# Kernel optimization log

Hardware: AMD Instinct MI355X
Metric: run time of the kernel (lower is better)

Reference implementation:

```python
import jax, jax.numpy as jnp
import numpy as np

H = 32          # num attention heads
KVH = 8         # num kv heads
D = 64          # head dim
HID = 2048      # hidden size
MAXB = 1024     # max_bias_length
BASE = 10000.0  # rope theta


def _rope(x, pos):
    # x: (B, S, h, D), pos: (S,) -- GPT-NeoX half-split rotary
    half = D // 2
    inv_freq = 1.0 / (BASE ** (jnp.arange(0, D, 2, dtype=jnp.float32) / D))  # (half,)
    ang = pos[:, None].astype(jnp.float32) * inv_freq                         # (S, half)
    cos = jnp.cos(ang)[None, :, None, :]
    sin = jnp.sin(ang)[None, :, None, :]
    x1, x2 = x[..., :half], x[..., half:]
    return jnp.concatenate([x1 * cos - x2 * sin, x2 * cos + x1 * sin], axis=-1)


def setup_inputs() -> dict:
    key = jax.random.key(0)
    ks = jax.random.split(key, 7)
    B, S = 2, 1024
    hidden_states = jax.random.normal(ks[0], (B, S, HID), dtype=jnp.float32)
    attention_mask = jnp.broadcast_to(
        jnp.tril(jnp.ones((S, S), dtype=jnp.int32))[None, None], (B, 1, S, S))
    # weights stored as (in, out): y = x @ W  (same math as torch Linear)
    Wq = jax.random.normal(ks[1], (HID, H * D), dtype=jnp.float32) * 0.02
    Wk = jax.random.normal(ks[2], (HID, KVH * D), dtype=jnp.float32) * 0.02
    Wv = jax.random.normal(ks[3], (HID, KVH * D), dtype=jnp.float32) * 0.02
    Wo = jax.random.normal(ks[4], (H * D, HID), dtype=jnp.float32) * 0.02
    bias_diag = jax.random.normal(ks[5], (H, MAXB), dtype=jnp.float32) * 0.001
    softmax_offset = jnp.zeros((H,), dtype=jnp.float32)
    return {"hidden_states": hidden_states, "attention_mask": attention_mask,
            "Wq": Wq, "Wk": Wk, "Wv": Wv, "Wo": Wo,
            "bias_diag": bias_diag, "softmax_offset": softmax_offset}


def reference(hidden_states, attention_mask, Wq, Wk, Wv, Wo, bias_diag, softmax_offset):
    B, S, _ = hidden_states.shape
    scaling = D ** (-0.5)
    pos = jnp.arange(S)

    q = (hidden_states @ Wq).reshape(B, S, H, D)
    k = (hidden_states @ Wk).reshape(B, S, KVH, D)
    v = (hidden_states @ Wv).reshape(B, S, KVH, D)

    q = _rope(q, pos)
    k = _rope(k, pos)

    # (B, H, S, D); repeat_kv via repeat on head axis
    q = q.transpose(0, 2, 1, 3)
    k = jnp.repeat(k.transpose(0, 2, 1, 3), H // KVH, axis=1)
    v = jnp.repeat(v.transpose(0, 2, 1, 3), H // KVH, axis=1)

    scores = jnp.einsum('bhqd,bhkd->bhqk', q, k) * scaling

    # learnable diagonal relative-position bias
    rel = pos[:, None] - pos[None, :]                     # (S, S)
    valid = ((rel >= 0) & (rel < MAXB)).astype(scores.dtype)
    idx = jnp.clip(rel, 0, MAXB - 1)
    bias = bias_diag[:, idx] * valid                      # (H, S, S)
    scores = scores + bias[None]

    scores = jnp.where(attention_mask[:, :, :, :S] == 0, -jnp.inf, scores)

    weights = jax.nn.softmax(scores.astype(jnp.float32), axis=-1)

    # adaptive offset subtraction + relu
    offset = jnp.abs(softmax_offset + 1.0)[None, :, None, None]
    num_visible = (pos + 1).astype(jnp.float32)[None, None, :, None]  # along query dim
    weights = jax.nn.relu(weights - offset / num_visible)

    attn_out = jnp.einsum('bhqk,bhkd->bhqd', weights.astype(v.dtype), v)
    attn_out = attn_out.transpose(0, 2, 1, 3).reshape(B, S, H * D)
    return attn_out @ Wo
```

## Files before the change

kernel.cpp:

```cpp
#include <hip/hip_runtime.h>
#include <cstdint>
#include <cstddef>

#define BB   2
#define SS   1024
#define HID  2048
#define HH   32
#define KVHH 8
#define DD   64
#define NQKV 3072
#define QKW  2560

typedef __attribute__((ext_vector_type(8))) short bf16x8;
typedef __attribute__((ext_vector_type(4))) float f32x4;
typedef __attribute__((ext_vector_type(4))) unsigned int u32x4;

__device__ __forceinline__ unsigned short f2bf(float f) {
    unsigned int u = __float_as_uint(f);
    unsigned int r = (u + 0x7fffu + ((u >> 16) & 1u)) >> 16;
    return (unsigned short)r;
}

__device__ __forceinline__ void g2l16(const unsigned short* g, unsigned short* l) {
    __builtin_amdgcn_global_load_lds(
        (__attribute__((address_space(1))) void*)(unsigned short*)g,
        (__attribute__((address_space(3))) void*)l,
        16, 0, 0);
}

__global__ __launch_bounds__(256) void prep(
    const float* __restrict__ hidden,
    const float* __restrict__ Wq, const float* __restrict__ Wk,
    const float* __restrict__ Wv, const float* __restrict__ Wo,
    unsigned short* __restrict__ hidden_bf,
    unsigned short* __restrict__ WqkvT,
    unsigned short* __restrict__ WoT)
{
    const int z   = blockIdx.z;
    const int tid = threadIdx.x;

    if (z == 4) {
        int r0 = blockIdx.y * 64, c0 = blockIdx.x * 64;
        #pragma unroll
        for (int p = 0; p < 4; ++p) {
            int f = tid + p * 256;
            int row = r0 + (f >> 4), c4 = c0 + (f & 15) * 4;
            float4 v = *(const float4*)&hidden[(size_t)row * 2048 + c4];
            ushort4 o;
            o.x = f2bf(v.x); o.y = f2bf(v.y); o.z = f2bf(v.z); o.w = f2bf(v.w);
            *(ushort4*)&hidden_bf[(size_t)row * 2048 + c4] = o;
        }
        return;
    }

    const float* W;
    unsigned short* Wt;
    int N;
    if (z == 0)      { W = Wq; Wt = WqkvT;                        N = 2048; }
    else if (z == 1) { W = Wk; Wt = WqkvT + (size_t)2048 * 2048;  N = 512;  }
    else if (z == 2) { W = Wv; Wt = WqkvT + (size_t)2560 * 2048;  N = 512;  }
    else             { W = Wo; Wt = WoT;                          N = 2048; }
    if (blockIdx.x * 64 >= N) return;

    __shared__ float t[64][68];
    const int n0 = blockIdx.x * 64, k0 = blockIdx.y * 64;
    #pragma unroll
    for (int p = 0; p < 4; ++p) {
        int f = tid + p * 256;
        int row = f >> 4, c4 = (f & 15) * 4;
        float4 v = *(const float4*)&W[(size_t)(k0 + row) * N + n0 + c4];
        t[row][c4 + 0] = v.x; t[row][c4 + 1] = v.y;
        t[row][c4 + 2] = v.z; t[row][c4 + 3] = v.w;
    }
    __syncthreads();
    #pragma unroll
    for (int p = 0; p < 4; ++p) {
        int f = tid + p * 256;
        int nrow = f >> 4, kc4 = (f & 15) * 4;
        ushort4 o;
        o.x = f2bf(t[kc4 + 0][nrow]);
        o.y = f2bf(t[kc4 + 1][nrow]);
        o.z = f2bf(t[kc4 + 2][nrow]);
        o.w = f2bf(t[kc4 + 3][nrow]);
        *(ushort4*)&Wt[(size_t)(n0 + nrow) * 2048 + k0 + kc4] = o;
    }
}

__global__ __launch_bounds__(256) void gemm_qkv_fused(
    const unsigned short* __restrict__ A,
    const unsigned short* __restrict__ Bt,
    unsigned short* __restrict__ qk_bf,
    unsigned short* __restrict__ v_t)
{
    __shared__ __align__(16) char smem[49152];
    float* Ctf = (float*)smem;

    const int tid  = threadIdx.x;
    const int lane = tid & 63;
    const int wave = tid >> 6;
    const int quad = lane >> 4;
    const int l15  = lane & 15;
    const int wm = (wave >> 1) * 64, wn = (wave & 1) * 32;
    const int m0 = blockIdx.y * 128, n0 = blockIdx.x * 64;
    const int K = 2048;

    f32x4 acc[4][2] = {};

#define STAGE_Q(k0s, buf) do {                                                \
    unsigned short* Ad = (unsigned short*)(smem + (buf) * 24576);             \
    unsigned short* Bd = (unsigned short*)(smem + (buf) * 24576 + 16384);     \
    _Pragma("unroll")                                                         \
    for (int p = 0; p < 4; ++p) {                                             \
        int ci = tid + p * 256;                                               \
        int row_ = ci >> 3, sc_ = (ci & 7) ^ (row_ & 7);                      \
        g2l16(&A[(size_t)(m0 + row_) * K + (k0s) + sc_ * 8], Ad + ci * 8);    \
    }                                                                         \
    _Pragma("unroll")                                                         \
    for (int p = 0; p < 2; ++p) {                                             \
        int ci = tid + p * 256;                                               \
        int row_ = ci >> 3, sc_ = (ci & 7) ^ (row_ & 7);                      \
        g2l16(&Bt[(size_t)(n0 + row_) * K + (k0s) + sc_ * 8], Bd + ci * 8);   \
    } } while (0)

    STAGE_Q(0, 0);
    __syncthreads();
    int cur = 0;
    for (int k0 = 0; k0 < K; k0 += 64) {
        if (k0 + 64 < K) STAGE_Q(k0 + 64, cur ^ 1);
        const short* Ab = (const short*)(smem + cur * 24576);
        const short* Bb = (const short*)(smem + cur * 24576 + 16384);

        #pragma unroll
        for (int s = 0; s < 2; ++s) {
            bf16x8 af[4], bfr[2];
            #pragma unroll
            for (int i = 0; i < 4; ++i) {
                int row = wm + i * 16 + l15;
                af[i] = *(const bf16x8*)(Ab + row * 64 +
                        ((((s << 2) | quad) ^ (row & 7)) * 8));
            }
            #pragma unroll
            for (int j = 0; j < 2; ++j) {
                int row = wn + j * 16 + l15;
                bfr[j] = *(const bf16x8*)(Bb + row * 64 +
                        ((((s << 2) | quad) ^ (row & 7)) * 8));
            }
            #pragma unroll
            for (int i = 0; i < 4; ++i)
                #pragma unroll
                for (int j = 0; j < 2; ++j)
                    acc[i][j] = __builtin_amdgcn_mfma_f32_16x16x32_bf16(
                        af[i], bfr[j], acc[i][j], 0, 0, 0);
        }
        __syncthreads();
        cur ^= 1;
    }

    #pragma unroll
    for (int i = 0; i < 4; ++i)
        #pragma unroll
        for (int j = 0; j < 2; ++j)
            #pragma unroll
            for (int rg = 0; rg < 4; ++rg)
                Ctf[(wm + i * 16 + quad * 4 + rg) * 65 + wn + j * 16 + l15]
                    = acc[i][j][rg];
    __syncthreads();

    const int bx = blockIdx.x;
    const int b  = m0 >> 10;
    const int s0 = m0 & 1023;

    if (bx < 40) {
        const int hc = bx * 64;
        const float scale = (bx < 32) ? 0.125f : 1.0f;
        #pragma unroll
        for (int p = 0; p < 4; ++p) {
            int idx = tid + p * 256;
            int row = idx >> 3, t0 = (idx & 7) * 4;
            int s = s0 + row;
            ushort4 o1, o2;
            #pragma unroll
            for (int k = 0; k < 4; ++k) {
                int t = t0 + k;
                float x1 = Ctf[row * 65 + t];
                float x2 = Ctf[row * 65 + t + 32];
                float inv = __expf(-(float)t * 0.28782313662425572f);
                float ang = (float)s * inv;
                float c  = __cosf(ang);
                float sn = __sinf(ang);
                ((unsigned short*)&o1)[k] = f2bf((x1 * c - x2 * sn) * scale);
                ((unsigned short*)&o2)[k] = f2bf((x2 * c + x1 * sn) * scale);
            }
            unsigned short* dst = qk_bf + (size_t)(m0 + row) * QKW + hc;
            *(ushort4*)&dst[t0]      = o1;
            *(ushort4*)&dst[t0 + 32] = o2;
        }
    } else {
        const int vb = b * 512 + (bx - 40) * 64;
        #pragma unroll
        for (int p = 0; p < 8; ++p) {
            int idx = tid + p * 256;
            int c = idx >> 5, srow = (idx & 31) * 4;
            ushort4 o;
            #pragma unroll
            for (int k = 0; k < 4; ++k)
                ((unsigned short*)&o)[k] = f2bf(Ctf[(srow + k) * 65 + c]);
            *(ushort4*)&v_t[(size_t)(vb + c) * 1024 + s0 + srow] = o;
        }
    }
#undef STAGE_Q
}

__global__ __launch_bounds__(256) void gemm_bf16_bt(
    const unsigned short* __restrict__ A,
    const unsigned short* __restrict__ Bt,
    float* __restrict__ C, int M, int N, int K)
{
    __shared__ __align__(16) char smem[49152];

    const int tid  = threadIdx.x;
    const int lane = tid & 63;
    const int wave = tid >> 6;
    const int quad = lane >> 4;
    const int l15  = lane & 15;
    const int wm = (wave >> 1) * 64, wn = (wave & 1) * 32;
    const int m0 = blockIdx.y * 128, n0 = blockIdx.x * 64;

    f32x4 acc[4][2] = {};

#define STAGE_O(k0s, buf) do {                                                \
    unsigned short* Ad = (unsigned short*)(smem + (buf) * 24576);             \
    unsigned short* Bd = (unsigned short*)(smem + (buf) * 24576 + 16384);     \
    _Pragma("unroll")                                                         \
    for (int p = 0; p < 4; ++p) {                                             \
        int ci = tid + p * 256;                                               \
        int row_ = ci >> 3, sc_ = (ci & 7) ^ (row_ & 7);                      \
        g2l16(&A[(size_t)(m0 + row_) * K + (k0s) + sc_ * 8], Ad + ci * 8);    \
    }                                                                         \
    _Pragma("unroll")                                                         \
    for (int p = 0; p < 2; ++p) {                                             \
        int ci = tid + p * 256;                                               \
        int row_ = ci >> 3, sc_ = (ci & 7) ^ (row_ & 7);                      \
        g2l16(&Bt[(size_t)(n0 + row_) * K + (k0s) + sc_ * 8], Bd + ci * 8);   \
    } } while (0)

    STAGE_O(0, 0);
    __syncthreads();
    int cur = 0;
    for (int k0 = 0; k0 < K; k0 += 64) {
        if (k0 + 64 < K) STAGE_O(k0 + 64, cur ^ 1);
        const short* Ab = (const short*)(smem + cur * 24576);
        const short* Bb = (const short*)(smem + cur * 24576 + 16384);

        #pragma unroll
        for (int s = 0; s < 2; ++s) {
            bf16x8 af[4], bfr[2];
            #pragma unroll
            for (int i = 0; i < 4; ++i) {
                int row = wm + i * 16 + l15;
                af[i] = *(const bf16x8*)(Ab + row * 64 +
                        ((((s << 2) | quad) ^ (row & 7)) * 8));
            }
            #pragma unroll
            for (int j = 0; j < 2; ++j) {
                int row = wn + j * 16 + l15;
                bfr[j] = *(const bf16x8*)(Bb + row * 64 +
                        ((((s << 2) | quad) ^ (row & 7)) * 8));
            }
            #pragma unroll
            for (int i = 0; i < 4; ++i)
                #pragma unroll
                for (int j = 0; j < 2; ++j)
                    acc[i][j] = __builtin_amdgcn_mfma_f32_16x16x32_bf16(
                        af[i], bfr[j], acc[i][j], 0, 0, 0);
        }
        __syncthreads();
        cur ^= 1;
    }

    #pragma unroll
    for (int i = 0; i < 4; ++i) {
        int grow = m0 + wm + i * 16 + quad * 4;
        #pragma unroll
        for (int j = 0; j < 2; ++j) {
            int gcol = n0 + wn + j * 16 + l15;
            #pragma unroll
            for (int rg = 0; rg < 4; ++rg)
                C[(size_t)(grow + rg) * N + gcol] = acc[i][j][rg];
        }
    }
#undef STAGE_O
}

__global__ __launch_bounds__(512, 4) void attn_mfma(
    const unsigned short* __restrict__ qk_bf,
    const unsigned short* __restrict__ v_t,
    const float* __restrict__ bias_diag,
    const float* __restrict__ soff,
    unsigned short* __restrict__ AO)
{
    const int id = (int)blockIdx.x;
    const int h  = id & 31;
    const int b  = (id >> 5) & 1;
    const int pi = id >> 6;
    const int kh = h >> 2;
    const int tid  = threadIdx.x;
    const int lane = tid & 63;
    const int wave = tid >> 6;
    const int grp  = wave >> 2;
    const int w4   = wave & 3;
    const int gt   = tid & 255;
    const int quad = lane >> 4;
    const int l15  = lane & 15;

    __shared__ short Ks[2][2][4096];
    __shared__ short Vs[2][2][4096];
    __shared__ float bd_s[1024];
    __shared__ float red[2][64];

    for (int i = tid; i < 1024; i += 512) bd_s[i] = bias_diag[h * 1024 + i];

    const unsigned short* Kg = qk_bf + (size_t)(b * SS) * QKW + 2048 + kh * 64;
    const unsigned short* Vg = v_t + (size_t)(b * 512 + kh * 64) * SS;

    short* KsG = &Ks[grp][0][0];
    short* VsG = &Vs[grp][0][0];
    float* Fred = (float*)&Ks[1][0][0];

#define STAGE_K(j, buf) do {                                                  \
    _Pragma("unroll")                                                         \
    for (int p = 0; p < 2; ++p) {                                             \
        int ci = gt + p * 256;                                                \
        int row_ = ci >> 3;                                                   \
        int sc_  = (ci & 7) ^ (row_ & 7);                                     \
        g2l16(Kg + (size_t)((j) * 64 + row_) * QKW + sc_ * 8,                 \
              (unsigned short*)(KsG + (buf) * 4096 + ci * 8));                \
    } } while (0)

#define STAGE_V(j, buf) do {                                                  \
    _Pragma("unroll")                                                         \
    for (int p = 0; p < 2; ++p) {                                             \
        int ci = gt + p * 256;                                                \
        int row_ = ci >> 3;                                                   \
        int sc_  = (ci & 7) ^ (row_ & 7);                                     \
        g2l16(Vg + (size_t)row_ * SS + (j) * 64 + sc_ * 8,                    \
              (unsigned short*)(VsG + (buf) * 4096 + ci * 8));                \
    } } while (0)

    #pragma unroll 1
    for (int half = 0; half < 2; ++half) {
        const int qt = half ? pi : 15 - pi;
        const int q0 = qt * 64;
        const int nI = (qt + 2) >> 1;
        const int qrow = q0 + w4 * 16 + l15;

        const unsigned short* Qg =
            qk_bf + (size_t)(b * SS + q0 + w4 * 16) * QKW + h * 64;
        bf16x8 qf0 = *(const bf16x8*)(Qg + (size_t)l15 * QKW + quad * 8);
        bf16x8 qf1 = *(const bf16x8*)(Qg + (size_t)l15 * QKW + 32 + quad * 8);

        float lpa[4] = {0.f, 0.f, 0.f, 0.f};
        if (grp <= qt) STAGE_K(grp, 0);
        __syncthreads();
        int cur = 0;
        for (int i = 0; i < nI; ++i) {
            const int j = 2 * i + grp;
            if (j + 2 <= qt) STAGE_K(j + 2, cur ^ 1);
            if (j <= qt) {
                const short* Kb = KsG + cur * 4096;
                const bool diag = (j == qt);
                f32x4 acc[4] = {};
                #pragma unroll
                for (int nb = 0; nb < 4; ++nb) {
                    if (diag && nb > w4) continue;
                    int row = nb * 16 + l15, sw = row & 7;
                    bf16x8 a0 = *(const bf16x8*)(Kb + row * 64 + ((quad ^ sw) * 8));
                    bf16x8 a1 = *(const bf16x8*)(Kb + row * 64 + (((quad + 4) ^ sw) * 8));
                    acc[nb] = __builtin_amdgcn_mfma_f32_16x16x32_bf16(a0, qf0, acc[nb], 0, 0, 0);
                    acc[nb] = __builtin_amdgcn_mfma_f32_16x16x32_bf16(a1, qf1, acc[nb], 0, 0, 0);
                }
                if (!diag) {
                    #pragma unroll
                    for (int nb = 0; nb < 4; ++nb) {
                        int rel0 = qrow - (j * 64 + nb * 16 + quad * 4);
                        #pragma unroll
                        for (int r = 0; r < 4; ++r)
                            lpa[r] += __expf(acc[nb][r] + bd_s[rel0 - r]);
                    }
                } else {
                    #pragma unroll
                    for (int nb = 0; nb < 4; ++nb) {
                        if (nb > w4) continue;
                        #pragma unroll
                        for (int r = 0; r < 4; ++r) {
                            int rel = qrow - (j * 64 + nb * 16 + quad * 4 + r);
                            if (rel >= 0) lpa[r] += __expf(acc[nb][r] + bd_s[rel]);
                        }
                    }
                }
            }
            __syncthreads();
            cur ^= 1;
        }

        float lp = (lpa[0] + lpa[1]) + (lpa[2] + lpa[3]);
        lp += __shfl_xor(lp, 16, 64);
        lp += __shfl_xor(lp, 32, 64);
        if (quad == 0) red[grp][w4 * 16 + l15] = lp;
        __syncthreads();
        lp = red[0][w4 * 16 + l15] + red[1][w4 * 16 + l15];
        const float invl = 1.f / lp;
        const float cl   = fabsf(soff[h] + 1.f) / (float)(qrow + 1) * lp;

        f32x4 oacc[4] = {};
        if (grp <= qt) { STAGE_K(grp, 0); STAGE_V(grp, 0); }
        __syncthreads();
        cur = 0;
        for (int i = 0; i < nI; ++i) {
            const int j = 2 * i + grp;
            if (j + 2 <= qt) { STAGE_K(j + 2, cur ^ 1); STAGE_V(j + 2, cur ^ 1); }
            if (j <= qt) {
                const short* Kb = KsG + cur * 4096;
                const short* Vb = VsG + cur * 4096;
                const bool diag = (j == qt);

                f32x4 acc[4] = {};
                #pragma unroll
                for (int nb = 0; nb < 4; ++nb) {
                    if (diag && nb > w4) continue;
                    int row = nb * 16 + l15, sw = row & 7;
                    bf16x8 a0 = *(const bf16x8*)(Kb + row * 64 + ((quad ^ sw) * 8));
                    bf16x8 a1 = *(const bf16x8*)(Kb + row * 64 + (((quad + 4) ^ sw) * 8));
                    acc[nb] = __builtin_amdgcn_mfma_f32_16x16x32_bf16(a0, qf0, acc[nb], 0, 0, 0);
                    acc[nb] = __builtin_amdgcn_mfma_f32_16x16x32_bf16(a1, qf1, acc[nb], 0, 0, 0);
                }

                unsigned int pk[4][2];
                if (!diag) {
                    #pragma unroll
                    for (int nb = 0; nb < 4; ++nb) {
                        float w[4];
                        int rel0 = qrow - (j * 64 + nb * 16 + quad * 4);
                        #pragma unroll
                        for (int r = 0; r < 4; ++r)
                            w[r] = fmaxf(__expf(acc[nb][r] + bd_s[rel0 - r]) - cl, 0.f);
                        asm("v_cvt_pk_bf16_f32 %0, %1, %2" : "=v"(pk[nb][0]) : "v"(w[0]), "v"(w[1]));
                        asm("v_cvt_pk_bf16_f32 %0, %1, %2" : "=v"(pk[nb][1]) : "v"(w[2]), "v"(w[3]));
                    }
                } else {
                    #pragma unroll
                    for (int nb = 0; nb < 4; ++nb) {
                        float w[4];
                        #pragma unroll
                        for (int r = 0; r < 4; ++r) {
                            int rel = qrow - (j * 64 + nb * 16 + quad * 4 + r);
                            float e = 0.f;
                            if (rel >= 0)
                                e = fmaxf(__expf(acc[nb][r] + bd_s[rel]) - cl, 0.f);
                            w[r] = e;
                        }
                        asm("v_cvt_pk_bf16_f32 %0, %1, %2" : "=v"(pk[nb][0]) : "v"(w[0]), "v"(w[1]));
                        asm("v_cvt_pk_bf16_f32 %0, %1, %2" : "=v"(pk[nb][1]) : "v"(w[2]), "v"(w[3]));
                    }
                }
                unsigned int ppk[4][2];
                #pragma unroll
                for (int nb = 0; nb < 4; ++nb) {
                    ppk[nb][0] = __shfl_xor(pk[nb][0], 16, 64);
                    ppk[nb][1] = __shfl_xor(pk[nb][1], 16, 64);
                }

                const bool oddq = quad & 1;
                const int  cv   = ((quad & 1) << 1) | (quad >> 1);
                #pragma unroll
                for (int s = 0; s < 2; ++s) {
                    if (diag && s == 1 && w4 < 2) continue;
                    unsigned int w0 = oddq ? ppk[2 * s + 1][0] : pk[2 * s][0];
                    unsigned int w1 = oddq ? ppk[2 * s + 1][1] : pk[2 * s][1];
                    unsigned int w2 = oddq ? pk[2 * s + 1][0]  : ppk[2 * s][0];
                    unsigned int w3 = oddq ? pk[2 * s + 1][1]  : ppk[2 * s][1];
                    u32x4 t; t[0] = w0; t[1] = w1; t[2] = w2; t[3] = w3;
                    bf16x8 pf = __builtin_bit_cast(bf16x8, t);
                    #pragma unroll
                    for (int nd = 0; nd < 4; ++nd) {
                        int rowv = nd * 16 + l15, swv = rowv & 7;
                        bf16x8 vf = *(const bf16x8*)(Vb + rowv * 64 + (((cv + 4 * s) ^ swv) * 8));
                        oacc[nd] = __builtin_amdgcn_mfma_f32_16x16x32_bf16(pf, vf, oacc[nd], 0, 0, 0);
                    }
                }
            }
            __syncthreads();
            cur ^= 1;
        }

        if (grp == 1) {
            #pragma unroll
            for (int nd = 0; nd < 4; ++nd)
                #pragma unroll
                for (int r = 0; r < 4; ++r)
                    Fred[(w4 * 16 + quad * 4 + r) * 64 + nd * 16 + l15] = oacc[nd][r];
        }
        __syncthreads();
        if (grp == 0) {
            float invl_r[4];
            #pragma unroll
            for (int r = 0; r < 4; ++r)
                invl_r[r] = __shfl(invl, quad * 4 + r, 64);
            unsigned short* aop =
                AO + (size_t)(b * SS + q0 + w4 * 16 + quad * 4) * 2048 + h * 64 + l15;
            #pragma unroll
            for (int nd = 0; nd < 4; ++nd)
                #pragma unroll
                for (int r = 0; r < 4; ++r) {
                    float o = (oacc[nd][r] +
                               Fred[(w4 * 16 + quad * 4 + r) * 64 + nd * 16 + l15])
                              * invl_r[r];
                    aop[(size_t)r * 2048 + nd * 16] = f2bf(o);
                }
        }
        __syncthreads();
    }
#undef STAGE_K
#undef STAGE_V
}

extern "C" void kernel_launch(void* const* d_in, const int* in_sizes, int n_in,
                              void* d_out, int out_size, void* d_ws, size_t ws_size,
                              hipStream_t stream)
{
    const float* hidden    = (const float*)d_in[0];
    const float* Wq        = (const float*)d_in[2];
    const float* Wk        = (const float*)d_in[3];
    const float* Wv        = (const float*)d_in[4];
    const float* Wo        = (const float*)d_in[5];
    const float* bias_diag = (const float*)d_in[6];
    const float* soff      = (const float*)d_in[7];
    float* out = (float*)d_out;

    char* wsb = (char*)d_ws;
    unsigned short* hidden_bf = (unsigned short*)wsb;
    unsigned short* WqkvT     = (unsigned short*)(wsb + (size_t)8388608);
    unsigned short* AO_bf     = (unsigned short*)(wsb + (size_t)12582912);
    unsigned short* WoT       = (unsigned short*)(wsb + (size_t)20971520);
    unsigned short* qk_bf     = (unsigned short*)(wsb + (size_t)29360128);
    unsigned short* v_t       = (unsigned short*)(wsb + (size_t)29360128 + (size_t)2048 * 2560 * 2);

    prep<<<dim3(32, 32, 5), dim3(256), 0, stream>>>(
        hidden, Wq, Wk, Wv, Wo, hidden_bf, WqkvT, WoT);

    gemm_qkv_fused<<<dim3(48, 16), dim3(256), 0, stream>>>(
        hidden_bf, WqkvT, qk_bf, v_t);

    attn_mfma<<<dim3(512), dim3(512), 0, stream>>>(
        qk_bf, v_t, bias_diag, soff, AO_bf);

    gemm_bf16_bt<<<dim3(2048 / 64, 2048 / 128), dim3(256), 0, stream>>>(
        AO_bf, WoT, out, 2048, 2048, 2048);
}
```

Baseline: 203.2 us.

## Split attention work per query tile and switch softmax to base-2 exp

```diff
diff --git a/kernel.cpp b/kernel.cpp
--- a/kernel.cpp
+++ b/kernel.cpp
@@ -19,6 +19,10 @@
     unsigned int u = __float_as_uint(f);
     unsigned int r = (u + 0x7fffu + ((u >> 16) & 1u)) >> 16;
     return (unsigned short)r;
+}
+
+__device__ __forceinline__ float ex2(float x) {
+    float r; asm("v_exp_f32 %0, %1" : "=v"(r) : "v"(x)); return r;
 }
 
 __device__ __forceinline__ void g2l16(const unsigned short* g, unsigned short* l) {
@@ -172,7 +176,7 @@
 
     if (bx < 40) {
         const int hc = bx * 64;
-        const float scale = (bx < 32) ? 0.125f : 1.0f;
+        const float scale = (bx < 32) ? 0.18033688011112042f : 1.0f;
         #pragma unroll
         for (int p = 0; p < 4; ++p) {
             int idx = tid + p * 256;
@@ -292,233 +296,221 @@
 #undef STAGE_O
 }
 
-__global__ __launch_bounds__(512, 4) void attn_mfma(
+__global__ __launch_bounds__(512, 8) void attn_mfma(
     const unsigned short* __restrict__ qk_bf,
     const unsigned short* __restrict__ v_t,
     const float* __restrict__ bias_diag,
     const float* __restrict__ soff,
     unsigned short* __restrict__ AO)
 {
+    static const unsigned char qtab[16] =
+        {15, 14, 13, 12, 10, 11, 8, 9, 4, 5, 6, 7, 1, 0, 3, 2};
     const int id = (int)blockIdx.x;
-    const int h  = id & 31;
-    const int b  = (id >> 5) & 1;
-    const int pi = id >> 6;
+    const int vq = id >> 8;
+    const int c  = id & 255;
+    const int qt = qtab[(vq << 2) | (c & 3)];
+    const int bh = c >> 2;
+    const int h  = bh & 31;
+    const int b  = bh >> 5;
     const int kh = h >> 2;
     const int tid  = threadIdx.x;
     const int lane = tid & 63;
     const int wave = tid >> 6;
     const int grp  = wave >> 2;
     const int w4   = wave & 3;
-    const int gt   = tid & 255;
     const int quad = lane >> 4;
     const int l15  = lane & 15;
-
-    __shared__ short Ks[2][2][4096];
-    __shared__ short Vs[2][2][4096];
+    const int q0   = qt * 64;
+
+    __shared__ short Ks[2][4096];
+    __shared__ short Vs[2][4096];
     __shared__ float bd_s[1024];
     __shared__ float red[2][64];
-
-    for (int i = tid; i < 1024; i += 512) bd_s[i] = bias_diag[h * 1024 + i];
+    float* Fred = (float*)&Ks[0][0];
+
+    for (int i = tid; i < 1024; i += 512)
+        bd_s[i] = bias_diag[h * 1024 + i] * 1.4426950408889634f;
 
     const unsigned short* Kg = qk_bf + (size_t)(b * SS) * QKW + 2048 + kh * 64;
     const unsigned short* Vg = v_t + (size_t)(b * 512 + kh * 64) * SS;
 
-    short* KsG = &Ks[grp][0][0];
-    short* VsG = &Vs[grp][0][0];
-    float* Fred = (float*)&Ks[1][0][0];
+    const int qrow = q0 + w4 * 16 + l15;
+
+    const unsigned short* Qg =
+        qk_bf + (size_t)(b * SS + q0 + w4 * 16) * QKW + h * 64;
+    bf16x8 qf0 = *(const bf16x8*)(Qg + (size_t)l15 * QKW + quad * 8);
+    bf16x8 qf1 = *(const bf16x8*)(Qg + (size_t)l15 * QKW + 32 + quad * 8);
 
 #define STAGE_K(j, buf) do {                                                  \
-    _Pragma("unroll")                                                         \
-    for (int p = 0; p < 2; ++p) {                                             \
-        int ci = gt + p * 256;                                                \
-        int row_ = ci >> 3;                                                   \
-        int sc_  = (ci & 7) ^ (row_ & 7);                                     \
-        g2l16(Kg + (size_t)((j) * 64 + row_) * QKW + sc_ * 8,                 \
-              (unsigned short*)(KsG + (buf) * 4096 + ci * 8));                \
-    } } while (0)
+    int ci = tid;                                                             \
+    int row_ = ci >> 3, sc_ = (ci & 7) ^ (row_ & 7);                          \
+    g2l16(Kg + (size_t)((j) * 64 + row_) * QKW + sc_ * 8,                     \
+          (unsigned short*)&Ks[buf][ci * 8]);                                 \
+} while (0)
 
 #define STAGE_V(j, buf) do {                                                  \
-    _Pragma("unroll")                                                         \
-    for (int p = 0; p < 2; ++p) {                                             \
-        int ci = gt + p * 256;                                                \
-        int row_ = ci >> 3;                                                   \
-        int sc_  = (ci & 7) ^ (row_ & 7);                                     \
-        g2l16(Vg + (size_t)row_ * SS + (j) * 64 + sc_ * 8,                    \
-              (unsigned short*)(VsG + (buf) * 4096 + ci * 8));                \
-    } } while (0)
-
-    #pragma unroll 1
-    for (int half = 0; half < 2; ++half) {
-        const int qt = half ? pi : 15 - pi;
-        const int q0 = qt * 64;
-        const int nI = (qt + 2) >> 1;
-        const int qrow = q0 + w4 * 16 + l15;
-
-        const unsigned short* Qg =
-            qk_bf + (size_t)(b * SS + q0 + w4 * 16) * QKW + h * 64;
-        bf16x8 qf0 = *(const bf16x8*)(Qg + (size_t)l15 * QKW + quad * 8);
-        bf16x8 qf1 = *(const bf16x8*)(Qg + (size_t)l15 * QKW + 32 + quad * 8);
-
-        float lpa[4] = {0.f, 0.f, 0.f, 0.f};
-        if (grp <= qt) STAGE_K(grp, 0);
-        __syncthreads();
-        int cur = 0;
-        for (int i = 0; i < nI; ++i) {
-            const int j = 2 * i + grp;
-            if (j + 2 <= qt) STAGE_K(j + 2, cur ^ 1);
-            if (j <= qt) {
-                const short* Kb = KsG + cur * 4096;
-                const bool diag = (j == qt);
-                f32x4 acc[4] = {};
-                #pragma unroll
-                for (int nb = 0; nb < 4; ++nb) {
-                    if (diag && nb > w4) continue;
-                    int row = nb * 16 + l15, sw = row & 7;
-                    bf16x8 a0 = *(const bf16x8*)(Kb + row * 64 + ((quad ^ sw) * 8));
-                    bf16x8 a1 = *(const bf16x8*)(Kb + row * 64 + (((quad + 4) ^ sw) * 8));
-                    acc[nb] = __builtin_amdgcn_mfma_f32_16x16x32_bf16(a0, qf0, acc[nb], 0, 0, 0);
-                    acc[nb] = __builtin_amdgcn_mfma_f32_16x16x32_bf16(a1, qf1, acc[nb], 0, 0, 0);
-                }
-                if (!diag) {
-                    #pragma unroll
-                    for (int nb = 0; nb < 4; ++nb) {
-                        int rel0 = qrow - (j * 64 + nb * 16 + quad * 4);
-                        #pragma unroll
-                        for (int r = 0; r < 4; ++r)
-                            lpa[r] += __expf(acc[nb][r] + bd_s[rel0 - r]);
-                    }
-                } else {
-                    #pragma unroll
-                    for (int nb = 0; nb < 4; ++nb) {
-                        if (nb > w4) continue;
-                        #pragma unroll
-                        for (int r = 0; r < 4; ++r) {
-                            int rel = qrow - (j * 64 + nb * 16 + quad * 4 + r);
-                            if (rel >= 0) lpa[r] += __expf(acc[nb][r] + bd_s[rel]);
-                        }
-                    }
-                }
-            }
-            __syncthreads();
-            cur ^= 1;
-        }
-
-        float lp = (lpa[0] + lpa[1]) + (lpa[2] + lpa[3]);
-        lp += __shfl_xor(lp, 16, 64);
-        lp += __shfl_xor(lp, 32, 64);
-        if (quad == 0) red[grp][w4 * 16 + l15] = lp;
-        __syncthreads();
-        lp = red[0][w4 * 16 + l15] + red[1][w4 * 16 + l15];
-        const float invl = 1.f / lp;
-        const float cl   = fabsf(soff[h] + 1.f) / (float)(qrow + 1) * lp;
-
-        f32x4 oacc[4] = {};
-        if (grp <= qt) { STAGE_K(grp, 0); STAGE_V(grp, 0); }
-        __syncthreads();
-        cur = 0;
-        for (int i = 0; i < nI; ++i) {
-            const int j = 2 * i + grp;
-            if (j + 2 <= qt) { STAGE_K(j + 2, cur ^ 1); STAGE_V(j + 2, cur ^ 1); }
-            if (j <= qt) {
-                const short* Kb = KsG + cur * 4096;
-                const short* Vb = VsG + cur * 4096;
-                const bool diag = (j == qt);
-
-                f32x4 acc[4] = {};
-                #pragma unroll
-                for (int nb = 0; nb < 4; ++nb) {
-                    if (diag && nb > w4) continue;
-                    int row = nb * 16 + l15, sw = row & 7;
-                    bf16x8 a0 = *(const bf16x8*)(Kb + row * 64 + ((quad ^ sw) * 8));
-                    bf16x8 a1 = *(const bf16x8*)(Kb + row * 64 + (((quad + 4) ^ sw) * 8));
-                    acc[nb] = __builtin_amdgcn_mfma_f32_16x16x32_bf16(a0, qf0, acc[nb], 0, 0, 0);
-                    acc[nb] = __builtin_amdgcn_mfma_f32_16x16x32_bf16(a1, qf1, acc[nb], 0, 0, 0);
-                }
-
-                unsigned int pk[4][2];
-                if (!diag) {
-                    #pragma unroll
-                    for (int nb = 0; nb < 4; ++nb) {
-                        float w[4];
-                        int rel0 = qrow - (j * 64 + nb * 16 + quad * 4);
-                        #pragma unroll
-                        for (int r = 0; r < 4; ++r)
-                            w[r] = fmaxf(__expf(acc[nb][r] + bd_s[rel0 - r]) - cl, 0.f);
-                        asm("v_cvt_pk_bf16_f32 %0, %1, %2" : "=v"(pk[nb][0]) : "v"(w[0]), "v"(w[1]));
-                        asm("v_cvt_pk_bf16_f32 %0, %1, %2" : "=v"(pk[nb][1]) : "v"(w[2]), "v"(w[3]));
-                    }
-                } else {
-                    #pragma unroll
-                    for (int nb = 0; nb < 4; ++nb) {
-                        float w[4];
-                        #pragma unroll
-                        for (int r = 0; r < 4; ++r) {
-                            int rel = qrow - (j * 64 + nb * 16 + quad * 4 + r);
-                            float e = 0.f;
-                            if (rel >= 0)
-                                e = fmaxf(__expf(acc[nb][r] + bd_s[rel]) - cl, 0.f);
-                            w[r] = e;
-                        }
-                        asm("v_cvt_pk_bf16_f32 %0, %1, %2" : "=v"(pk[nb][0]) : "v"(w[0]), "v"(w[1]));
-                        asm("v_cvt_pk_bf16_f32 %0, %1, %2" : "=v"(pk[nb][1]) : "v"(w[2]), "v"(w[3]));
-                    }
-                }
-                unsigned int ppk[4][2];
-                #pragma unroll
-                for (int nb = 0; nb < 4; ++nb) {
-                    ppk[nb][0] = __shfl_xor(pk[nb][0], 16, 64);
-                    ppk[nb][1] = __shfl_xor(pk[nb][1], 16, 64);
-                }
-
-                const bool oddq = quad & 1;
-                const int  cv   = ((quad & 1) << 1) | (quad >> 1);
-                #pragma unroll
-                for (int s = 0; s < 2; ++s) {
-                    if (diag && s == 1 && w4 < 2) continue;
-                    unsigned int w0 = oddq ? ppk[2 * s + 1][0] : pk[2 * s][0];
-                    unsigned int w1 = oddq ? ppk[2 * s + 1][1] : pk[2 * s][1];
-                    unsigned int w2 = oddq ? pk[2 * s + 1][0]  : ppk[2 * s][0];
-                    unsigned int w3 = oddq ? pk[2 * s + 1][1]  : ppk[2 * s][1];
-                    u32x4 t; t[0] = w0; t[1] = w1; t[2] = w2; t[3] = w3;
-                    bf16x8 pf = __builtin_bit_cast(bf16x8, t);
-                    #pragma unroll
-                    for (int nd = 0; nd < 4; ++nd) {
-                        int rowv = nd * 16 + l15, swv = rowv & 7;
-                        bf16x8 vf = *(const bf16x8*)(Vb + rowv * 64 + (((cv + 4 * s) ^ swv) * 8));
-                        oacc[nd] = __builtin_amdgcn_mfma_f32_16x16x32_bf16(pf, vf, oacc[nd], 0, 0, 0);
-                    }
-                }
-            }
-            __syncthreads();
-            cur ^= 1;
-        }
-
-        if (grp == 1) {
-            #pragma unroll
-            for (int nd = 0; nd < 4; ++nd)
+    int ci = tid;                                                             \
+    int row_ = ci >> 3, sc_ = (ci & 7) ^ (row_ & 7);                          \
+    g2l16(Vg + (size_t)row_ * SS + (j) * 64 + sc_ * 8,                        \
+          (unsigned short*)&Vs[buf][ci * 8]);                                 \
+} while (0)
+
+    float lpa[4] = {0.f, 0.f, 0.f, 0.f};
+    STAGE_K(0, 0);
+    __syncthreads();
+    int cur = 0;
+    for (int j = 0; j <= qt; ++j) {
+        if (j < qt) STAGE_K(j + 1, cur ^ 1);
+        const short* Kb = Ks[cur];
+        const bool diag = (j == qt);
+
+        f32x4 acc[2] = {};
+        #pragma unroll
+        for (int nn = 0; nn < 2; ++nn) {
+            int nb = 2 * grp + nn;
+            if (diag && nb > w4) continue;
+            int row = nb * 16 + l15, sw = row & 7;
+            bf16x8 a0 = *(const bf16x8*)(Kb + row * 64 + ((quad ^ sw) * 8));
+            bf16x8 a1 = *(const bf16x8*)(Kb + row * 64 + (((quad + 4) ^ sw) * 8));
+            acc[nn] = __builtin_amdgcn_mfma_f32_16x16x32_bf16(a0, qf0, acc[nn], 0, 0, 0);
+            acc[nn] = __builtin_amdgcn_mfma_f32_16x16x32_bf16(a1, qf1, acc[nn], 0, 0, 0);
+        }
+        if (!diag) {
+            #pragma unroll
+            for (int nn = 0; nn < 2; ++nn) {
+                int rel0 = qrow - (j * 64 + (2 * grp + nn) * 16 + quad * 4);
                 #pragma unroll
                 for (int r = 0; r < 4; ++r)
-                    Fred[(w4 * 16 + quad * 4 + r) * 64 + nd * 16 + l15] = oacc[nd][r];
-        }
-        __syncthreads();
-        if (grp == 0) {
-            float invl_r[4];
-            #pragma unroll
-            for (int r = 0; r < 4; ++r)
-                invl_r[r] = __shfl(invl, quad * 4 + r, 64);
-            unsigned short* aop =
-                AO + (size_t)(b * SS + q0 + w4 * 16 + quad * 4) * 2048 + h * 64 + l15;
-            #pragma unroll
-            for (int nd = 0; nd < 4; ++nd)
+                    lpa[r] += ex2(acc[nn][r] + bd_s[rel0 - r]);
+            }
+        } else {
+            #pragma unroll
+            for (int nn = 0; nn < 2; ++nn) {
+                int nb = 2 * grp + nn;
+                if (nb > w4) continue;
                 #pragma unroll
                 for (int r = 0; r < 4; ++r) {
-                    float o = (oacc[nd][r] +
-                               Fred[(w4 * 16 + quad * 4 + r) * 64 + nd * 16 + l15])
-                              * invl_r[r];
-                    aop[(size_t)r * 2048 + nd * 16] = f2bf(o);
+                    int rel = qrow - (j * 64 + nb * 16 + quad * 4 + r);
+                    if (rel >= 0) lpa[r] += ex2(acc[nn][r] + bd_s[rel]);
                 }
+            }
         }
         __syncthreads();
+        cur ^= 1;
+    }
+
+    float lp = (lpa[0] + lpa[1]) + (lpa[2] + lpa[3]);
+    lp += __shfl_xor(lp, 16, 64);
+    lp += __shfl_xor(lp, 32, 64);
+    if (quad == 0) red[grp][w4 * 16 + l15] = lp;
+    __syncthreads();
+    lp = red[0][w4 * 16 + l15] + red[1][w4 * 16 + l15];
+    const float invl = 1.f / lp;
+    const float cl   = fabsf(soff[h] + 1.f) / (float)(qrow + 1) * lp;
+
+    f32x4 oacc[4] = {};
+    STAGE_K(0, 0);
+    STAGE_V(0, 0);
+    __syncthreads();
+    cur = 0;
+    for (int j = 0; j <= qt; ++j) {
+        if (j < qt) { STAGE_K(j + 1, cur ^ 1); STAGE_V(j + 1, cur ^ 1); }
+        const short* Kb = Ks[cur];
+        const short* Vb = Vs[cur];
+        const bool diag = (j == qt);
+
+        f32x4 acc[2] = {};
+        #pragma unroll
+        for (int nn = 0; nn < 2; ++nn) {
+            int nb = 2 * grp + nn;
+            if (diag && nb > w4) continue;
+            int row = nb * 16 + l15, sw = row & 7;
+            bf16x8 a0 = *(const bf16x8*)(Kb + row * 64 + ((quad ^ sw) * 8));
+            bf16x8 a1 = *(const bf16x8*)(Kb + row * 64 + (((quad + 4) ^ sw) * 8));
+            acc[nn] = __builtin_amdgcn_mfma_f32_16x16x32_bf16(a0, qf0, acc[nn], 0, 0, 0);
+            acc[nn] = __builtin_amdgcn_mfma_f32_16x16x32_bf16(a1, qf1, acc[nn], 0, 0, 0);
+        }
+
+        unsigned int pk[2][2];
+        if (!diag) {
+            #pragma unroll
+            for (int nn = 0; nn < 2; ++nn) {
+                float w[4];
+                int rel0 = qrow - (j * 64 + (2 * grp + nn) * 16 + quad * 4);
+                #pragma unroll
+                for (int r = 0; r < 4; ++r)
+                    w[r] = fmaxf(ex2(acc[nn][r] + bd_s[rel0 - r]) - cl, 0.f);
+                asm("v_cvt_pk_bf16_f32 %0, %1, %2" : "=v"(pk[nn][0]) : "v"(w[0]), "v"(w[1]));
+                asm("v_cvt_pk_bf16_f32 %0, %1, %2" : "=v"(pk[nn][1]) : "v"(w[2]), "v"(w[3]));
+            }
+        } else {
+            #pragma unroll
+            for (int nn = 0; nn < 2; ++nn) {
+                int nb = 2 * grp + nn;
+                float w[4];
+                #pragma unroll
+                for (int r = 0; r < 4; ++r) {
+                    int rel = qrow - (j * 64 + nb * 16 + quad * 4 + r);
+                    float e = 0.f;
+                    if (rel >= 0)
+                        e = fmaxf(ex2(acc[nn][r] + bd_s[rel]) - cl, 0.f);
+                    w[r] = e;
+                }
+                asm("v_cvt_pk_bf16_f32 %0, %1, %2" : "=v"(pk[nn][0]) : "v"(w[0]), "v"(w[1]));
+                asm("v_cvt_pk_bf16_f32 %0, %1, %2" : "=v"(pk[nn][1]) : "v"(w[2]), "v"(w[3]));
+            }
+        }
+        unsigned int ppk[2][2];
+        #pragma unroll
+        for (int nn = 0; nn < 2; ++nn) {
+            ppk[nn][0] = __shfl_xor(pk[nn][0], 16, 64);
+            ppk[nn][1] = __shfl_xor(pk[nn][1], 16, 64);
+        }
+
+        if (!(diag && grp == 1 && w4 < 2)) {
+            const bool oddq = quad & 1;
+            const int  cv   = ((quad & 1) << 1) | (quad >> 1);
+            unsigned int w0 = oddq ? ppk[1][0] : pk[0][0];
+            unsigned int w1 = oddq ? ppk[1][1] : pk[0][1];
+            unsigned int w2 = oddq ? pk[1][0]  : ppk[0][0];
+            unsigned int w3 = oddq ? pk[1][1]  : ppk[0][1];
+            u32x4 t; t[0] = w0; t[1] = w1; t[2] = w2; t[3] = w3;
+            bf16x8 pf = __builtin_bit_cast(bf16x8, t);
+            #pragma unroll
+            for (int nd = 0; nd < 4; ++nd) {
+                int rowv = nd * 16 + l15, swv = rowv & 7;
+                bf16x8 vf = *(const bf16x8*)(Vb + rowv * 64 + (((cv + 4 * grp) ^ swv) * 8));
+                oacc[nd] = __builtin_amdgcn_mfma_f32_16x16x32_bf16(pf, vf, oacc[nd], 0, 0, 0);
+            }
+        }
+        __syncthreads();
+        cur ^= 1;
+    }
+
+    if (grp == 1) {
+        #pragma unroll
+        for (int nd = 0; nd < 4; ++nd)
+            #pragma unroll
+            for (int r = 0; r < 4; ++r)
+                Fred[(w4 * 16 + quad * 4 + r) * 64 + nd * 16 + l15] = oacc[nd][r];
+    }
+    __syncthreads();
+    if (grp == 0) {
+        float invl_r[4];
+        #pragma unroll
+        for (int r = 0; r < 4; ++r)
+            invl_r[r] = __shfl(invl, quad * 4 + r, 64);
+        unsigned short* aop =
+            AO + (size_t)(b * SS + q0 + w4 * 16 + quad * 4) * 2048 + h * 64 + l15;
+        #pragma unroll
+        for (int nd = 0; nd < 4; ++nd)
+            #pragma unroll
+            for (int r = 0; r < 4; ++r) {
+                float o = (oacc[nd][r] +
+                           Fred[(w4 * 16 + quad * 4 + r) * 64 + nd * 16 + l15])
+                          * invl_r[r];
+                aop[(size_t)r * 2048 + nd * 16] = f2bf(o);
+            }
     }
 #undef STAGE_K
 #undef STAGE_V
@@ -551,7 +543,7 @@
     gemm_qkv_fused<<<dim3(48, 16), dim3(256), 0, stream>>>(
         hidden_bf, WqkvT, qk_bf, v_t);
 
-    attn_mfma<<<dim3(512), dim3(512), 0, stream>>>(
+    attn_mfma<<<dim3(1024), dim3(512), 0, stream>>>(
         qk_bf, v_t, bias_diag, soff, AO_bf);
 
     gemm_bf16_bt<<<dim3(2048 / 64, 2048 / 128), dim3(256), 0, stream>>>(
```

Measured after the change: 197.1 us, median of 2. 1.03x faster.
